# Kernel tuning notes

Measured on AMD Instinct MI355X. Metric: run time of the kernel, lower is better.

## Reference

```python
import jax, jax.numpy as jnp
import numpy as np

B, D, DM, K, KA = 4096, 64, 256, 32, 16


def setup_inputs() -> dict:
    key = jax.random.key(0)
    ks = jax.random.split(key, 20)
    rn = lambda i, shape, s=1.0: jax.random.normal(ks[i], shape, dtype=jnp.float32) * s
    return dict(
        z=rn(0, (B, D)),
        rw=jax.random.uniform(ks[1], (B, K), dtype=jnp.float32),
        action_z=rn(2, (B, D)),
        action_rw=jax.random.uniform(ks[3], (B, KA), dtype=jnp.float32),
        action_code_z=rn(4, (B, D)),
        control=rn(5, (B, D)),
        exact_covector=rn(6, (B, D)),
        chart_emb=rn(7, (K, DM), 0.05),
        chart_anchor=rn(8, (K, D)),
        action_chart_emb=rn(9, (KA, DM), 0.05),
        action_chart_anchor=rn(10, (KA, D)),
        z_embed_W=rn(11, (D, DM), 0.05), z_embed_b=jnp.zeros((DM,), jnp.float32),
        lat_W=rn(12, (D, DM), 0.05), lat_b=jnp.zeros((DM,), jnp.float32),
        code_W=rn(13, (D, DM), 0.05), code_b=jnp.zeros((DM,), jnp.float32),
        Wq=rn(14, (DM, DM), 0.05), Wk=rn(15, (DM, DM), 0.05),
        Wv=rn(16, (DM, DM), 0.05), Wo=rn(17, (DM, DM), 0.05),
        form_W=rn(18, (DM, D), 0.05), form_b=jnp.zeros((D,), jnp.float32),
    )


def _spectral_linear(x, W, b):
    # SpectralLinear: weight normalized by its largest singular value.
    sigma = jnp.linalg.svd(W, compute_uv=False)[0]
    return x @ (W / jnp.maximum(sigma, jnp.float32(1e-8))) + b


def _forward(z, rw, action_z, action_rw, action_code_z, control, exact_covector,
             chart_emb, chart_anchor, action_chart_emb, action_chart_anchor,
             z_embed_W, z_embed_b, lat_W, lat_b, code_W, code_b,
             Wq, Wk, Wv, Wo, form_W, form_b):
    b = z.shape[0]
    # ChartTokenizer: routing-weighted chart embeddings + anchor latents.
    chart_x = rw[:, :, None] * chart_emb[None]                      # [B,K,DM]
    chart_z = jnp.broadcast_to(chart_anchor[None], (b, K, D))       # [B,K,D]
    a_chart_x = action_rw[:, :, None] * action_chart_emb[None]      # [B,KA,DM]
    a_chart_z = jnp.broadcast_to(action_chart_anchor[None], (b, KA, D))
    # LatentTokenizers: single token per latent.
    lat_x = (action_z @ lat_W + lat_b)[:, None, :]                  # [B,1,DM]
    code_x = (action_code_z @ code_W + code_b)[:, None, :]          # [B,1,DM]
    ctx_x = jnp.concatenate([lat_x, code_x, a_chart_x, chart_x], axis=1)   # [B,S,DM]
    ctx_z = jnp.concatenate([action_z[:, None], action_code_z[:, None], a_chart_z, chart_z], axis=1)  # [B,S,D]
    # CovariantAttention (1 head): feature scores biased by latent-space distance.
    x_q = z @ z_embed_W + z_embed_b                                 # [B,DM]
    q = x_q @ Wq                                                    # [B,DM]
    k = jnp.einsum('bsd,de->bse', ctx_x, Wk)                        # [B,S,DM]
    v = jnp.einsum('bsd,de->bse', ctx_x, Wv)
    dist2 = jnp.sum((z[:, None, :] - ctx_z) ** 2, axis=-1)          # [B,S]
    scores = jnp.einsum('bd,bsd->bs', q, k) / jnp.sqrt(jnp.float32(DM)) - dist2
    attn = jax.nn.softmax(scores, axis=-1)
    feat = jnp.einsum('bs,bsd->bd', attn, v) @ Wo                   # [B,DM]
    # Residual reward one-form, projected off the (detached) exact direction.
    form_raw = _spectral_linear(feat, form_W, form_b)               # [B,D]
    e = jax.lax.stop_gradient(exact_covector)
    e_norm2 = jnp.sum(e * e, axis=-1, keepdims=True)
    coeff = jnp.where(e_norm2 > 1e-8,
                      jnp.sum(form_raw * e, axis=-1, keepdims=True) / jnp.maximum(e_norm2, 1e-8),
                      jnp.zeros_like(e_norm2))
    form_cov = form_raw - coeff * e
    # Non-conservative scalar reward contribution.
    return jnp.sum(form_cov * control, axis=-1, keepdims=True)      # [B,1]


def reference(z, rw, action_z, action_rw, action_code_z, control, exact_covector,
              chart_emb, chart_anchor, action_chart_emb, action_chart_anchor,
              z_embed_W, z_embed_b, lat_W, lat_b, code_W, code_b,
              Wq, Wk, Wv, Wo, form_W, form_b):
    return _forward(z, rw, action_z, action_rw, action_code_z, control, exact_covector,
                    chart_emb, chart_anchor, action_chart_emb, action_chart_anchor,
                    z_embed_W, z_embed_b, lat_W, lat_b, code_W, code_b,
                    Wq, Wk, Wv, Wo, form_W, form_b)
```

## Files before the change

### kernel.cpp

```cpp
#include <hip/hip_runtime.h>

#define PITERS 96

#define OFF_XQ   0
#define OFF_KL   16640
#define OFF_KC   33280
#define OFF_VL   49920
#define OFF_VC   66560
#define OFF_KE   83200
#define OFF_VE   95488
#define OFF_M    107776
#define OFF_G    124160
#define OFF_PLm  128256
#define OFF_PLc  132416
#define OFF_PCm  132488
#define OFF_PCc  136648
#define OFF_CK2  136720
#define OFF_ANCT 139840
#define OFF_ANCN 142912
#define OFF_VM   142976
#define OFF_LM   146048
#define OFF_CM   150208
#define OFF_RS   154368

__device__ __forceinline__ float wred(float v) {
  #pragma unroll
  for (int m = 32; m >= 1; m >>= 1) v += __shfl_xor(v, m, 64);
  return v;
}

__global__ __launch_bounds__(256)
void k1a(const float* __restrict__ chemb, const float* __restrict__ aemb,
         const float* __restrict__ zW, const float* __restrict__ zb,
         const float* __restrict__ latW, const float* __restrict__ latb,
         const float* __restrict__ codeW, const float* __restrict__ codeb,
         const float* __restrict__ Wq, const float* __restrict__ Wk,
         const float* __restrict__ Wv, const float* __restrict__ Wo,
         const float* __restrict__ fW, float* __restrict__ ws) {
  __shared__ __align__(16) float red[1024];
  const int t = threadIdx.x, b = blockIdx.x;
  const int j = t & 63, ks = t >> 6;

  const float *a0p, *a1p, *a2p, *a3p;
  const float* Bm;
  int bstride = 256, jbase = 0;
  int d0, d1, d2, d3;
  bool gpath = false;

  if (b < 340) {
    int u = b / 68, r2 = b - u * 68;
    int rg = r2 >> 2, jc = r2 & 3; jbase = jc * 64;
    const float *Wmat, *bias;
    if (u == 0)      { Wmat = zW;    bias = zb;    Bm = Wq; }
    else if (u == 1) { Wmat = latW;  bias = latb;  Bm = Wk; }
    else if (u == 2) { Wmat = codeW; bias = codeb; Bm = Wk; }
    else if (u == 3) { Wmat = latW;  bias = latb;  Bm = Wv; }
    else             { Wmat = codeW; bias = codeb; Bm = Wv; }
    int r0 = rg * 4;
    int rr0 = r0 + 0, rr1 = r0 + 1, rr2 = r0 + 2, rr3 = r0 + 3;
    a0p = (rr0 < 64) ? (Wmat + rr0 * 256) : bias;
    a1p = (rr1 <= 64) ? ((rr1 < 64) ? (Wmat + rr1 * 256) : bias) : bias;
    a2p = (rr2 <= 64) ? ((rr2 < 64) ? (Wmat + rr2 * 256) : bias) : bias;
    a3p = (rr3 <= 64) ? ((rr3 < 64) ? (Wmat + rr3 * 256) : bias) : bias;
    d0 = u * 16640 + rr0 * 256 + jbase;
    d1 = (rr1 <= 64) ? (u * 16640 + rr1 * 256 + jbase) : -1;
    d2 = (rr2 <= 64) ? (u * 16640 + rr2 * 256 + jbase) : -1;
    d3 = (rr3 <= 64) ? (u * 16640 + rr3 * 256 + jbase) : -1;
  } else if (b < 436) {
    int b2 = b - 340; int isV = (b2 >= 48); int rr = b2 - (isV ? 48 : 0);
    int rg = rr >> 2, jc = rr & 3; jbase = jc * 64;
    Bm = isV ? Wv : Wk;
    int base = isV ? OFF_VE : OFF_KE;
    int s0 = rg * 4;
    const float* e0 = (s0 + 0 < 16) ? (aemb + (s0 + 0) * 256) : (chemb + (s0 + 0 - 16) * 256);
    const float* e1 = (s0 + 1 < 16) ? (aemb + (s0 + 1) * 256) : (chemb + (s0 + 1 - 16) * 256);
    const float* e2 = (s0 + 2 < 16) ? (aemb + (s0 + 2) * 256) : (chemb + (s0 + 2 - 16) * 256);
    const float* e3 = (s0 + 3 < 16) ? (aemb + (s0 + 3) * 256) : (chemb + (s0 + 3 - 16) * 256);
    a0p = e0; a1p = e1; a2p = e2; a3p = e3;
    d0 = base + (s0 + 0) * 256 + jbase;
    d1 = base + (s0 + 1) * 256 + jbase;
    d2 = base + (s0 + 2) * 256 + jbase;
    d3 = base + (s0 + 3) * 256 + jbase;
  } else if (b < 500) {
    int i0 = (b - 436) * 4;
    Bm = fW; bstride = 64;
    a0p = Wo + (i0 + 0) * 256; a1p = Wo + (i0 + 1) * 256;
    a2p = Wo + (i0 + 2) * 256; a3p = Wo + (i0 + 3) * 256;
    d0 = OFF_M + (i0 + 0) * 64; d1 = OFF_M + (i0 + 1) * 64;
    d2 = OFF_M + (i0 + 2) * 64; d3 = OFF_M + (i0 + 3) * 64;
  } else {
    gpath = true;
    int i0 = (b - 500) * 4;
    Bm = fW; bstride = 64;
    a0p = fW + i0 + 0; a1p = fW + i0 + 1; a2p = fW + i0 + 2; a3p = fW + i0 + 3;
    d0 = OFF_G + (i0 + 0) * 64; d1 = OFF_G + (i0 + 1) * 64;
    d2 = OFF_G + (i0 + 2) * 64; d3 = OFF_G + (i0 + 3) * 64;
  }

  float acc0 = 0.f, acc1 = 0.f, acc2 = 0.f, acc3 = 0.f;
  const float* bp = Bm + (ks * 64) * bstride + jbase + j;
  if (!gpath) {
    const float* a0 = a0p + ks * 64;
    const float* a1 = a1p + ks * 64;
    const float* a2 = a2p + ks * 64;
    const float* a3 = a3p + ks * 64;
    #pragma unroll 4
    for (int k4 = 0; k4 < 16; ++k4) {
      float b0 = bp[(k4 * 4 + 0) * bstride];
      float b1 = bp[(k4 * 4 + 1) * bstride];
      float b2 = bp[(k4 * 4 + 2) * bstride];
      float b3 = bp[(k4 * 4 + 3) * bstride];
      float4 x0 = *(const float4*)(a0 + k4 * 4);
      float4 x1 = *(const float4*)(a1 + k4 * 4);
      float4 x2 = *(const float4*)(a2 + k4 * 4);
      float4 x3 = *(const float4*)(a3 + k4 * 4);
      acc0 += x0.x * b0 + x0.y * b1 + x0.z * b2 + x0.w * b3;
      acc1 += x1.x * b0 + x1.y * b1 + x1.z * b2 + x1.w * b3;
      acc2 += x2.x * b0 + x2.y * b1 + x2.z * b2 + x2.w * b3;
      acc3 += x3.x * b0 + x3.y * b1 + x3.z * b2 + x3.w * b3;
    }
  } else {
    const float* a0 = a0p + (ks * 64) * 64;
    const float* a1 = a1p + (ks * 64) * 64;
    const float* a2 = a2p + (ks * 64) * 64;
    const float* a3 = a3p + (ks * 64) * 64;
    #pragma unroll 4
    for (int k = 0; k < 64; ++k) {
      float bv = bp[k * bstride];
      acc0 += a0[k * 64] * bv;
      acc1 += a1[k * 64] * bv;
      acc2 += a2[k * 64] * bv;
      acc3 += a3[k * 64] * bv;
    }
  }
  red[0 * 256 + t] = acc0;
  red[1 * 256 + t] = acc1;
  red[2 * 256 + t] = acc2;
  red[3 * 256 + t] = acc3;
  __syncthreads();
  if (t < 64) {
    if (d0 >= 0) ws[d0 + t] = (red[t] + red[64 + t]) + (red[128 + t] + red[192 + t]);
    if (d1 >= 0) ws[d1 + t] = (red[256 + t] + red[320 + t]) + (red[384 + t] + red[448 + t]);
    if (d2 >= 0) ws[d2 + t] = (red[512 + t] + red[576 + t]) + (red[640 + t] + red[704 + t]);
    if (d3 >= 0) ws[d3 + t] = (red[768 + t] + red[832 + t]) + (red[896 + t] + red[960 + t]);
  }
}

__global__ __launch_bounds__(256)
void k1b(const float* __restrict__ latb, const float* __restrict__ codeb,
         const float* __restrict__ aanc, const float* __restrict__ chanc,
         float* __restrict__ ws) {
  __shared__ __align__(16) float red[256];
  const int t = threadIdx.x, b = blockIdx.x;

  if (b == 0) {
    if (t >= 64) return;
    const int ln = t;
    float4 h[16];
    #pragma unroll
    for (int k4 = 0; k4 < 16; ++k4)
      h[k4] = *(const float4*)(ws + OFF_G + ln * 64 + k4 * 4);
    float rn = 0.f;
    #pragma unroll
    for (int k4 = 0; k4 < 16; ++k4)
      rn += h[k4].x * h[k4].x + h[k4].y * h[k4].y + h[k4].z * h[k4].z + h[k4].w * h[k4].w;
    float bv = rn; int bj = ln;
    #pragma unroll
    for (int m = 32; m >= 1; m >>= 1) {
      float ov = __shfl_xor(bv, m, 64);
      int   oj = __shfl_xor(bj, m, 64);
      if (ov > bv || (ov == bv && oj < bj)) { bv = ov; bj = oj; }
    }
    float v = ws[OFF_G + bj * 64 + ln];
    for (int it = 0; it < PITERS; ++it) {
      red[ln] = v;
      float y0 = 0.f, y1 = 0.f, y2 = 0.f, y3 = 0.f;
      #pragma unroll
      for (int k4 = 0; k4 < 16; ++k4) {
        float4 vv = *(const float4*)&red[k4 * 4];
        y0 = fmaf(h[k4].x, vv.x, y0);
        y1 = fmaf(h[k4].y, vv.y, y1);
        y2 = fmaf(h[k4].z, vv.z, y2);
        y3 = fmaf(h[k4].w, vv.w, y3);
      }
      float y = (y0 + y1) + (y2 + y3);
      if ((it & 7) == 7) {
        float n2 = wred(y * y);
        y = (n2 > 0.f) ? y * rsqrtf(n2) : 0.f;
      }
      v = y;
    }
    red[ln] = v;
    float y0 = 0.f, y1 = 0.f, y2 = 0.f, y3 = 0.f;
    #pragma unroll
    for (int k4 = 0; k4 < 16; ++k4) {
      float4 vv = *(const float4*)&red[k4 * 4];
      y0 = fmaf(h[k4].x, vv.x, y0);
      y1 = fmaf(h[k4].y, vv.y, y1);
      y2 = fmaf(h[k4].z, vv.z, y2);
      y3 = fmaf(h[k4].w, vv.w, y3);
    }
    float y = (y0 + y1) + (y2 + y3);
    float num = wred(v * y), den = wred(v * v);
    if (ln == 0) {
      float lam = (den > 1e-37f) ? num / den : 0.f;
      lam = fmaxf(lam, 0.f);
      ws[OFF_RS] = 1.f / fmaxf(sqrtf(lam), 1e-8f);
    }
    return;
  }

  const int q = b - 1;

  if (q == 374) {
    for (int e = t; e < 3072; e += 256) {
      int d = e / 48, s = e - d * 48;
      const float* a = (s < 16) ? (aanc + s * 64) : (chanc + (s - 16) * 64);
      ws[OFF_ANCT + e] = a[d];
    }
    if (t < 64) {
      float n = 0.f;
      if (t < 48) {
        const float* a = (t < 16) ? (aanc + t * 64) : (chanc + (t - 16) * 64);
        #pragma unroll 4
        for (int d = 0; d < 64; ++d) n += a[d] * a[d];
      }
      ws[OFF_ANCN + t] = n;
    }
    return;
  }
  if (q == 373) {
    if (t < 65) {
      const float* ap = ws + OFF_XQ + t * 256;
      const float* bp = ws + OFF_KL + 64 * 256;
      float acc = 0.f;
      #pragma unroll 4
      for (int e = 0; e < 256; ++e) acc += ap[e] * bp[e];
      ws[OFF_PLc + t] = acc;
    } else if (t >= 128 && t < 193) {
      int r = t - 128;
      const float* ap = ws + OFF_XQ + r * 256;
      const float* bp = ws + OFF_KC + 64 * 256;
      float acc = 0.f;
      #pragma unroll 4
      for (int e = 0; e < 256; ++e) acc += ap[e] * bp[e];
      ws[OFF_PCc + r] = acc;
    }
    return;
  }

  const int j = t & 63, ks = t >> 6;
  const float* ap; const float* bp;
  int bstride, dstBase, nout = 64;
  if (q < 325) {
    int g = q / 65, r = q - g * 65;
    const float* A = ws + ((g < 3) ? OFF_XQ : (g == 3 ? OFF_VL : OFF_VC)) + r * 256;
    if (g == 0)      { bp = ws + OFF_KL + j * 256 + ks * 64; bstride = 1; dstBase = OFF_PLm + r * 64; }
    else if (g == 1) { bp = ws + OFF_KC + j * 256 + ks * 64; bstride = 1; dstBase = OFF_PCm + r * 64; }
    else if (g == 2) { int jj = (j < 48) ? j : 47;
                       bp = ws + OFF_KE + jj * 256 + ks * 64; bstride = 1; dstBase = OFF_CK2 + r * 48; nout = 48; }
    else if (g == 3) { bp = ws + OFF_M + (ks * 64) * 64 + j; bstride = 64; dstBase = OFF_LM + r * 64; }
    else             { bp = ws + OFF_M + (ks * 64) * 64 + j; bstride = 64; dstBase = OFF_CM + r * 64; }
    ap = A + ks * 64;
  } else {
    int s = q - 325;
    ap = ws + OFF_VE + s * 256 + ks * 64;
    bp = ws + OFF_M + (ks * 64) * 64 + j; bstride = 64;
    dstBase = OFF_VM + s * 64;
  }
  float a0 = 0.f, a1 = 0.f, a2 = 0.f, a3 = 0.f;
  #pragma unroll 4
  for (int k = 0; k < 64; k += 4) {
    a0 += ap[k + 0] * bp[(k + 0) * bstride];
    a1 += ap[k + 1] * bp[(k + 1) * bstride];
    a2 += ap[k + 2] * bp[(k + 2) * bstride];
    a3 += ap[k + 3] * bp[(k + 3) * bstride];
  }
  red[t] = (a0 + a1) + (a2 + a3);
  __syncthreads();
  if (t < nout) ws[dstBase + t] = red[t] + red[64 + t] + red[128 + t] + red[192 + t];
}

__global__ __launch_bounds__(256)
void k2_main(const float* __restrict__ z, const float* __restrict__ rw,
             const float* __restrict__ az, const float* __restrict__ arw,
             const float* __restrict__ acz, const float* __restrict__ ctrl,
             const float* __restrict__ ecov, const float* __restrict__ fb,
             const float* __restrict__ ws, float* __restrict__ out) {
  const int t = threadIdx.x;
  const int wv = t >> 6, ln = t & 63;

  const int bb = blockIdx.x * 8 + wv * 2;
  float z0 = z[bb * 64 + ln],        z1 = z[(bb + 1) * 64 + ln];
  float a0 = az[bb * 64 + ln],       a1 = az[(bb + 1) * 64 + ln];
  float c0 = acz[bb * 64 + ln],      c1 = acz[(bb + 1) * 64 + ln];
  float cc0 = ctrl[bb * 64 + ln],    cc1 = ctrl[(bb + 1) * 64 + ln];
  float ee0 = ecov[bb * 64 + ln],    ee1 = ecov[(bb + 1) * 64 + ln];
  float fbv = fb[ln];
  const float rs = ws[OFF_RS];
  float fold0 = 1.f, fold1 = 1.f;
  if (ln < 16)      { fold0 = arw[bb * 16 + ln];        fold1 = arw[(bb + 1) * 16 + ln]; }
  else if (ln < 48) { fold0 = rw[bb * 32 + (ln - 16)];  fold1 = rw[(bb + 1) * 32 + (ln - 16)]; }

  float dL0 = wred((z0 - a0) * (z0 - a0));
  float dL1 = wred((z1 - a1) * (z1 - a1));
  float dC0 = wred((z0 - c0) * (z0 - c0));
  float dC1 = wred((z1 - c1) * (z1 - c1));
  float zn0 = wred(z0 * z0);
  float zn1 = wred(z1 * z1);

  const float* plm = ws + OFF_PLm + ln;
  const float* pcm = ws + OFF_PCm + ln;
  float uL0 = plm[64 * 64], uL1 = uL0;
  float uC0 = pcm[64 * 64], uC1 = uC0;
  #pragma unroll 8
  for (int k = 0; k < 64; ++k) {
    float pm = plm[k * 64], pc = pcm[k * 64];
    float zk0 = __shfl(z0, k, 64), zk1 = __shfl(z1, k, 64);
    uL0 = fmaf(zk0, pm, uL0); uL1 = fmaf(zk1, pm, uL1);
    uC0 = fmaf(zk0, pc, uC0); uC1 = fmaf(zk1, pc, uC1);
  }
  float plc = ws[OFF_PLc + ln], pcc = ws[OFF_PCc + ln];
  float plcc = ws[OFF_PLc + 64], pccc = ws[OFF_PCc + 64];
  float sL0 = wred(uL0 * a0 + z0 * plc) + plcc;
  float sL1 = wred(uL1 * a1 + z1 * plc) + plcc;
  float sC0 = wred(uC0 * c0 + z0 * pcc) + pccc;
  float sC1 = wred(uC1 * c1 + z1 * pcc) + pccc;
  float scl0 = sL0 * 0.0625f - dL0, scl1 = sL1 * 0.0625f - dL1;
  float scc0 = sC0 * 0.0625f - dC0, scc1 = sC1 * 0.0625f - dC1;

  const float* ck = ws + OFF_CK2 + ln;
  const float* an = ws + OFF_ANCT + ln;
  float ca0 = ck[64 * 48], ca1 = ca0;
  float za0 = 0.f, za1 = 0.f;
  #pragma unroll 8
  for (int k = 0; k < 64; ++k) {
    float cv = ck[k * 48], av = an[k * 48];
    float zk0 = __shfl(z0, k, 64), zk1 = __shfl(z1, k, 64);
    ca0 = fmaf(zk0, cv, ca0); ca1 = fmaf(zk1, cv, ca1);
    za0 = fmaf(zk0, av, za0); za1 = fmaf(zk1, av, za1);
  }
  float ancn = ws[OFF_ANCN + ln];
  float sc0 = fold0 * ca0 * 0.0625f - (zn0 - 2.f * za0 + ancn);
  float sc1 = fold1 * ca1 * 0.0625f - (zn1 - 2.f * za1 + ancn);
  if (ln == 48) { sc0 = scl0; sc1 = scl1; }
  if (ln == 49) { sc0 = scc0; sc1 = scc1; }
  if (ln > 49)  { sc0 = -1e30f; sc1 = -1e30f; }

  float mx0 = sc0, mx1 = sc1;
  #pragma unroll
  for (int m = 32; m >= 1; m >>= 1) {
    mx0 = fmaxf(mx0, __shfl_xor(mx0, m, 64));
    mx1 = fmaxf(mx1, __shfl_xor(mx1, m, 64));
  }
  float ev0 = (ln < 50) ? __expf(sc0 - mx0) : 0.f;
  float ev1 = (ln < 50) ? __expf(sc1 - mx1) : 0.f;
  float sum0 = wred(ev0), sum1 = wred(ev1);
  float w0 = ev0 * (1.f / sum0) * fold0;
  float w1 = ev1 * (1.f / sum1) * fold1;

  float g0 = 0.f, g1 = 0.f;
  const float* vm = ws + OFF_VM + ln;
  #pragma unroll 8
  for (int s = 0; s < 48; ++s) {
    float vvv = vm[s * 64];
    float s0 = __shfl(w0, s, 64), s1 = __shfl(w1, s, 64);
    g0 = fmaf(s0, vvv, g0); g1 = fmaf(s1, vvv, g1);
  }
  const float* lm = ws + OFF_LM + ln;
  const float* cm = ws + OFF_CM + ln;
  float l0 = lm[64 * 64], l1 = l0;
  float m0 = cm[64 * 64], m1 = m0;
  #pragma unroll 8
  for (int k = 0; k < 64; ++k) {
    float lv = lm[k * 64], cv = cm[k * 64];
    float ak0 = __shfl(a0, k, 64), ak1 = __shfl(a1, k, 64);
    float qk0 = __shfl(c0, k, 64), qk1 = __shfl(c1, k, 64);
    l0 = fmaf(ak0, lv, l0); l1 = fmaf(ak1, lv, l1);
    m0 = fmaf(qk0, cv, m0); m1 = fmaf(qk1, cv, m1);
  }
  float w48_0 = __shfl(w0, 48, 64), w49_0 = __shfl(w0, 49, 64);
  float w48_1 = __shfl(w1, 48, 64), w49_1 = __shfl(w1, 49, 64);
  g0 += w48_0 * l0 + w49_0 * m0;
  g1 += w48_1 * l1 + w49_1 * m1;

  #pragma unroll
  for (int s = 0; s < 2; ++s) {
    float g  = (s == 0) ? g0 : g1;
    float cc = (s == 0) ? cc0 : cc1;
    float ee = (s == 0) ? ee0 : ee1;
    int bbs  = bb + s;
    float gc = wred(g * cc);
    float ge = wred(g * ee);
    float ec = wred(ee * cc);
    float en = wred(ee * ee);
    float fc = wred(fbv * cc);
    float fe = wred(fbv * ee);
    if (ln == 0) {
      float A, Bv;
      if (en > 1e-8f) { float r = ec / en; A = gc - ge * r; Bv = fc - fe * r; }
      else { A = gc; Bv = fc; }
      out[bbs] = A * rs + Bv;
    }
  }
}

extern "C" void kernel_launch(void* const* d_in, const int* in_sizes, int n_in,
                              void* d_out, int out_size, void* d_ws, size_t ws_size,
                              hipStream_t stream) {
  const float* z     = (const float*)d_in[0];
  const float* rw    = (const float*)d_in[1];
  const float* az    = (const float*)d_in[2];
  const float* arw   = (const float*)d_in[3];
  const float* acz   = (const float*)d_in[4];
  const float* ctrl  = (const float*)d_in[5];
  const float* ecov  = (const float*)d_in[6];
  const float* chemb = (const float*)d_in[7];
  const float* chanc = (const float*)d_in[8];
  const float* aemb  = (const float*)d_in[9];
  const float* aanc  = (const float*)d_in[10];
  const float* zW    = (const float*)d_in[11];
  const float* zb    = (const float*)d_in[12];
  const float* latW  = (const float*)d_in[13];
  const float* latb  = (const float*)d_in[14];
  const float* codeW = (const float*)d_in[15];
  const float* codeb = (const float*)d_in[16];
  const float* Wq    = (const float*)d_in[17];
  const float* Wk    = (const float*)d_in[18];
  const float* Wv    = (const float*)d_in[19];
  const float* Wo    = (const float*)d_in[20];
  const float* fW    = (const float*)d_in[21];
  const float* fb    = (const float*)d_in[22];
  float* ws  = (float*)d_ws;
  float* out = (float*)d_out;

  k1a<<<516, 256, 0, stream>>>(chemb, aemb, zW, zb, latW, latb, codeW, codeb,
                               Wq, Wk, Wv, Wo, fW, ws);
  k1b<<<376, 256, 0, stream>>>(latb, codeb, aanc, chanc, ws);
  k2_main<<<512, 256, 0, stream>>>(z, rw, az, arw, acz, ctrl, ecov, fb, ws, out);
}
```

Measured before the change: 172.8 us.

## Compute spectral norm via repeated Gram squaring in one block, fewer power iterations

The Gram matrix fW^T fW is now computed inside a single k1a block in shared memory and then squared five times with trace normalisation, so the power method runs on G^32. That lets the power iteration drop from 96 steps to 6. The serial power-iteration block moves out of k1b into k1a, and the OFF_G workspace round trip disappears. The cost is that one k1a block now does several 64x64 matmuls serially and uses about 52KB of shared memory, which may lower occupancy for every k1a block. Accuracy now depends on the repeated squaring converging well.

```diff
diff --git a/kernel.cpp b/kernel.cpp
--- a/kernel.cpp
+++ b/kernel.cpp
@@ -1,6 +1,6 @@
 #include <hip/hip_runtime.h>
 
-#define PITERS 96
+#define PITERS 6
 
 #define OFF_XQ   0
 #define OFF_KL   16640
@@ -10,7 +10,6 @@
 #define OFF_KE   83200
 #define OFF_VE   95488
 #define OFF_M    107776
-#define OFF_G    124160
 #define OFF_PLm  128256
 #define OFF_PLc  132416
 #define OFF_PCm  132488
@@ -37,16 +36,152 @@
          const float* __restrict__ Wq, const float* __restrict__ Wk,
          const float* __restrict__ Wv, const float* __restrict__ Wo,
          const float* __restrict__ fW, float* __restrict__ ws) {
-  __shared__ __align__(16) float red[1024];
+  __shared__ __align__(16) float sm[13120];
   const int t = threadIdx.x, b = blockIdx.x;
+
+  if (b == 500) {
+    const int ln = t & 63;
+    float* bufA = sm;
+    float* G0   = sm + 4352;
+    float* bufB = sm + 8704;
+    float* red  = sm + 13056;
+    const int ty = t >> 4, tx = t & 15;
+    const int i0 = ty * 4, j0 = tx * 4;
+    float acc[4][4];
+    #pragma unroll
+    for (int i = 0; i < 4; ++i)
+      #pragma unroll
+      for (int j = 0; j < 4; ++j) acc[i][j] = 0.f;
+    for (int c = 0; c < 4; ++c) {
+      if (c) __syncthreads();
+      for (int e = t; e < 4096; e += 256) {
+        int k = e >> 6, i = e & 63;
+        bufA[i * 68 + k] = fW[(c * 64 + k) * 64 + i];
+      }
+      __syncthreads();
+      #pragma unroll 4
+      for (int k4 = 0; k4 < 16; ++k4) {
+        float4 av[4], bv[4];
+        #pragma unroll
+        for (int i = 0; i < 4; ++i) av[i] = *(const float4*)&bufA[(i0 + i) * 68 + k4 * 4];
+        #pragma unroll
+        for (int j = 0; j < 4; ++j) bv[j] = *(const float4*)&bufA[(j0 + j) * 68 + k4 * 4];
+        #pragma unroll
+        for (int i = 0; i < 4; ++i)
+          #pragma unroll
+          for (int j = 0; j < 4; ++j)
+            acc[i][j] += av[i].x * bv[j].x + av[i].y * bv[j].y + av[i].z * bv[j].z + av[i].w * bv[j].w;
+      }
+    }
+    if (ty == tx) red[ty] = acc[0][0] + acc[1][1] + acc[2][2] + acc[3][3];
+    __syncthreads();
+    {
+      float tr = 0.f;
+      #pragma unroll
+      for (int x = 0; x < 16; ++x) tr += red[x];
+      float inv = (tr > 0.f) ? 1.f / tr : 0.f;
+      #pragma unroll
+      for (int i = 0; i < 4; ++i) {
+        *(float4*)&G0[(i0 + i) * 68 + j0]   = make_float4(acc[i][0], acc[i][1], acc[i][2], acc[i][3]);
+        *(float4*)&bufB[(i0 + i) * 68 + j0] = make_float4(acc[i][0] * inv, acc[i][1] * inv,
+                                                          acc[i][2] * inv, acc[i][3] * inv);
+      }
+    }
+    __syncthreads();
+    float* src = bufB;
+    float* dst = bufA;
+    for (int sq = 0; sq < 5; ++sq) {
+      #pragma unroll
+      for (int i = 0; i < 4; ++i)
+        #pragma unroll
+        for (int j = 0; j < 4; ++j) acc[i][j] = 0.f;
+      #pragma unroll 4
+      for (int k4 = 0; k4 < 16; ++k4) {
+        float4 av[4], bv[4];
+        #pragma unroll
+        for (int i = 0; i < 4; ++i) av[i] = *(const float4*)&src[(i0 + i) * 68 + k4 * 4];
+        #pragma unroll
+        for (int j = 0; j < 4; ++j) bv[j] = *(const float4*)&src[(j0 + j) * 68 + k4 * 4];
+        #pragma unroll
+        for (int i = 0; i < 4; ++i)
+          #pragma unroll
+          for (int j = 0; j < 4; ++j)
+            acc[i][j] += av[i].x * bv[j].x + av[i].y * bv[j].y + av[i].z * bv[j].z + av[i].w * bv[j].w;
+      }
+      if (ty == tx) red[ty] = acc[0][0] + acc[1][1] + acc[2][2] + acc[3][3];
+      __syncthreads();
+      {
+        float tr = 0.f;
+        #pragma unroll
+        for (int x = 0; x < 16; ++x) tr += red[x];
+        float inv = (tr > 0.f) ? 1.f / tr : 0.f;
+        #pragma unroll
+        for (int i = 0; i < 4; ++i)
+          *(float4*)&dst[(i0 + i) * 68 + j0] = make_float4(acc[i][0] * inv, acc[i][1] * inv,
+                                                           acc[i][2] * inv, acc[i][3] * inv);
+      }
+      __syncthreads();
+      float* tmp = src; src = dst; dst = tmp;
+    }
+    if (t < 64) {
+      float4 h[16];
+      #pragma unroll
+      for (int k4 = 0; k4 < 16; ++k4) h[k4] = *(const float4*)&src[ln * 68 + k4 * 4];
+      float rn = 0.f;
+      #pragma unroll
+      for (int k4 = 0; k4 < 16; ++k4)
+        rn += h[k4].x * h[k4].x + h[k4].y * h[k4].y + h[k4].z * h[k4].z + h[k4].w * h[k4].w;
+      float bnv = rn; int bj = ln;
+      #pragma unroll
+      for (int m = 32; m >= 1; m >>= 1) {
+        float ov = __shfl_xor(bnv, m, 64);
+        int   oj = __shfl_xor(bj, m, 64);
+        if (ov > bnv || (ov == bnv && oj < bj)) { bnv = ov; bj = oj; }
+      }
+      float v = src[bj * 68 + ln];
+      for (int pi = 0; pi < PITERS; ++pi) {
+        red[ln] = v;
+        float y0 = 0.f, y1 = 0.f, y2 = 0.f, y3 = 0.f;
+        #pragma unroll
+        for (int k4 = 0; k4 < 16; ++k4) {
+          float4 vvv = *(const float4*)&red[k4 * 4];
+          y0 = fmaf(h[k4].x, vvv.x, y0);
+          y1 = fmaf(h[k4].y, vvv.y, y1);
+          y2 = fmaf(h[k4].z, vvv.z, y2);
+          y3 = fmaf(h[k4].w, vvv.w, y3);
+        }
+        float y = (y0 + y1) + (y2 + y3);
+        float n2 = wred(y * y);
+        v = (n2 > 0.f) ? y * rsqrtf(n2) : 0.f;
+      }
+      red[ln] = v;
+      float y0 = 0.f, y1 = 0.f, y2 = 0.f, y3 = 0.f;
+      #pragma unroll
+      for (int k4 = 0; k4 < 16; ++k4) {
+        float4 gg = *(const float4*)&G0[ln * 68 + k4 * 4];
+        float4 vvv = *(const float4*)&red[k4 * 4];
+        y0 = fmaf(gg.x, vvv.x, y0);
+        y1 = fmaf(gg.y, vvv.y, y1);
+        y2 = fmaf(gg.z, vvv.z, y2);
+        y3 = fmaf(gg.w, vvv.w, y3);
+      }
+      float y = (y0 + y1) + (y2 + y3);
+      float num = wred(v * y), den = wred(v * v);
+      if (ln == 0) {
+        float lam = (den > 1e-37f) ? num / den : 0.f;
+        lam = fmaxf(lam, 0.f);
+        ws[OFF_RS] = 1.f / fmaxf(sqrtf(lam), 1e-8f);
+      }
+    }
+    return;
+  }
+
+  float* red = sm;
   const int j = t & 63, ks = t >> 6;
-
   const float *a0p, *a1p, *a2p, *a3p;
   const float* Bm;
   int bstride = 256, jbase = 0;
   int d0, d1, d2, d3;
-  bool gpath = false;
-
   if (b < 340) {
     int u = b / 68, r2 = b - u * 68;
     int rg = r2 >> 2, jc = r2 & 3; jbase = jc * 64;
@@ -57,12 +192,12 @@
     else if (u == 3) { Wmat = latW;  bias = latb;  Bm = Wv; }
     else             { Wmat = codeW; bias = codeb; Bm = Wv; }
     int r0 = rg * 4;
-    int rr0 = r0 + 0, rr1 = r0 + 1, rr2 = r0 + 2, rr3 = r0 + 3;
-    a0p = (rr0 < 64) ? (Wmat + rr0 * 256) : bias;
-    a1p = (rr1 <= 64) ? ((rr1 < 64) ? (Wmat + rr1 * 256) : bias) : bias;
-    a2p = (rr2 <= 64) ? ((rr2 < 64) ? (Wmat + rr2 * 256) : bias) : bias;
-    a3p = (rr3 <= 64) ? ((rr3 < 64) ? (Wmat + rr3 * 256) : bias) : bias;
-    d0 = u * 16640 + rr0 * 256 + jbase;
+    int rr1 = r0 + 1, rr2 = r0 + 2, rr3 = r0 + 3;
+    a0p = (r0 < 64) ? (Wmat + r0 * 256) : bias;
+    a1p = (rr1 < 64) ? (Wmat + rr1 * 256) : bias;
+    a2p = (rr2 < 64) ? (Wmat + rr2 * 256) : bias;
+    a3p = (rr3 < 64) ? (Wmat + rr3 * 256) : bias;
+    d0 = u * 16640 + r0 * 256 + jbase;
     d1 = (rr1 <= 64) ? (u * 16640 + rr1 * 256 + jbase) : -1;
     d2 = (rr2 <= 64) ? (u * 16640 + rr2 * 256 + jbase) : -1;
     d3 = (rr3 <= 64) ? (u * 16640 + rr3 * 256 + jbase) : -1;
@@ -72,66 +207,42 @@
     Bm = isV ? Wv : Wk;
     int base = isV ? OFF_VE : OFF_KE;
     int s0 = rg * 4;
-    const float* e0 = (s0 + 0 < 16) ? (aemb + (s0 + 0) * 256) : (chemb + (s0 + 0 - 16) * 256);
-    const float* e1 = (s0 + 1 < 16) ? (aemb + (s0 + 1) * 256) : (chemb + (s0 + 1 - 16) * 256);
-    const float* e2 = (s0 + 2 < 16) ? (aemb + (s0 + 2) * 256) : (chemb + (s0 + 2 - 16) * 256);
-    const float* e3 = (s0 + 3 < 16) ? (aemb + (s0 + 3) * 256) : (chemb + (s0 + 3 - 16) * 256);
-    a0p = e0; a1p = e1; a2p = e2; a3p = e3;
+    a0p = (s0 + 0 < 16) ? (aemb + (s0 + 0) * 256) : (chemb + (s0 + 0 - 16) * 256);
+    a1p = (s0 + 1 < 16) ? (aemb + (s0 + 1) * 256) : (chemb + (s0 + 1 - 16) * 256);
+    a2p = (s0 + 2 < 16) ? (aemb + (s0 + 2) * 256) : (chemb + (s0 + 2 - 16) * 256);
+    a3p = (s0 + 3 < 16) ? (aemb + (s0 + 3) * 256) : (chemb + (s0 + 3 - 16) * 256);
     d0 = base + (s0 + 0) * 256 + jbase;
     d1 = base + (s0 + 1) * 256 + jbase;
     d2 = base + (s0 + 2) * 256 + jbase;
     d3 = base + (s0 + 3) * 256 + jbase;
-  } else if (b < 500) {
+  } else {
     int i0 = (b - 436) * 4;
     Bm = fW; bstride = 64;
     a0p = Wo + (i0 + 0) * 256; a1p = Wo + (i0 + 1) * 256;
     a2p = Wo + (i0 + 2) * 256; a3p = Wo + (i0 + 3) * 256;
     d0 = OFF_M + (i0 + 0) * 64; d1 = OFF_M + (i0 + 1) * 64;
     d2 = OFF_M + (i0 + 2) * 64; d3 = OFF_M + (i0 + 3) * 64;
-  } else {
-    gpath = true;
-    int i0 = (b - 500) * 4;
-    Bm = fW; bstride = 64;
-    a0p = fW + i0 + 0; a1p = fW + i0 + 1; a2p = fW + i0 + 2; a3p = fW + i0 + 3;
-    d0 = OFF_G + (i0 + 0) * 64; d1 = OFF_G + (i0 + 1) * 64;
-    d2 = OFF_G + (i0 + 2) * 64; d3 = OFF_G + (i0 + 3) * 64;
-  }
-
+  }
   float acc0 = 0.f, acc1 = 0.f, acc2 = 0.f, acc3 = 0.f;
   const float* bp = Bm + (ks * 64) * bstride + jbase + j;
-  if (!gpath) {
-    const float* a0 = a0p + ks * 64;
-    const float* a1 = a1p + ks * 64;
-    const float* a2 = a2p + ks * 64;
-    const float* a3 = a3p + ks * 64;
-    #pragma unroll 4
-    for (int k4 = 0; k4 < 16; ++k4) {
-      float b0 = bp[(k4 * 4 + 0) * bstride];
-      float b1 = bp[(k4 * 4 + 1) * bstride];
-      float b2 = bp[(k4 * 4 + 2) * bstride];
-      float b3 = bp[(k4 * 4 + 3) * bstride];
-      float4 x0 = *(const float4*)(a0 + k4 * 4);
-      float4 x1 = *(const float4*)(a1 + k4 * 4);
-      float4 x2 = *(const float4*)(a2 + k4 * 4);
-      float4 x3 = *(const float4*)(a3 + k4 * 4);
-      acc0 += x0.x * b0 + x0.y * b1 + x0.z * b2 + x0.w * b3;
-      acc1 += x1.x * b0 + x1.y * b1 + x1.z * b2 + x1.w * b3;
-      acc2 += x2.x * b0 + x2.y * b1 + x2.z * b2 + x2.w * b3;
-      acc3 += x3.x * b0 + x3.y * b1 + x3.z * b2 + x3.w * b3;
-    }
-  } else {
-    const float* a0 = a0p + (ks * 64) * 64;
-    const float* a1 = a1p + (ks * 64) * 64;
-    const float* a2 = a2p + (ks * 64) * 64;
-    const float* a3 = a3p + (ks * 64) * 64;
-    #pragma unroll 4
-    for (int k = 0; k < 64; ++k) {
-      float bv = bp[k * bstride];
-      acc0 += a0[k * 64] * bv;
-      acc1 += a1[k * 64] * bv;
-      acc2 += a2[k * 64] * bv;
-      acc3 += a3[k * 64] * bv;
-    }
+  const float* a0 = a0p + ks * 64;
+  const float* a1 = a1p + ks * 64;
+  const float* a2 = a2p + ks * 64;
+  const float* a3 = a3p + ks * 64;
+  #pragma unroll 4
+  for (int k4 = 0; k4 < 16; ++k4) {
+    float b0 = bp[(k4 * 4 + 0) * bstride];
+    float b1 = bp[(k4 * 4 + 1) * bstride];
+    float b2 = bp[(k4 * 4 + 2) * bstride];
+    float b3 = bp[(k4 * 4 + 3) * bstride];
+    float4 x0 = *(const float4*)(a0 + k4 * 4);
+    float4 x1 = *(const float4*)(a1 + k4 * 4);
+    float4 x2 = *(const float4*)(a2 + k4 * 4);
+    float4 x3 = *(const float4*)(a3 + k4 * 4);
+    acc0 += x0.x * b0 + x0.y * b1 + x0.z * b2 + x0.w * b3;
+    acc1 += x1.x * b0 + x1.y * b1 + x1.z * b2 + x1.w * b3;
+    acc2 += x2.x * b0 + x2.y * b1 + x2.z * b2 + x2.w * b3;
+    acc3 += x3.x * b0 + x3.y * b1 + x3.z * b2 + x3.w * b3;
   }
   red[0 * 256 + t] = acc0;
   red[1 * 256 + t] = acc1;
@@ -150,67 +261,8 @@
 void k1b(const float* __restrict__ latb, const float* __restrict__ codeb,
          const float* __restrict__ aanc, const float* __restrict__ chanc,
          float* __restrict__ ws) {
-  __shared__ __align__(16) float red[256];
-  const int t = threadIdx.x, b = blockIdx.x;
-
-  if (b == 0) {
-    if (t >= 64) return;
-    const int ln = t;
-    float4 h[16];
-    #pragma unroll
-    for (int k4 = 0; k4 < 16; ++k4)
-      h[k4] = *(const float4*)(ws + OFF_G + ln * 64 + k4 * 4);
-    float rn = 0.f;
-    #pragma unroll
-    for (int k4 = 0; k4 < 16; ++k4)
-      rn += h[k4].x * h[k4].x + h[k4].y * h[k4].y + h[k4].z * h[k4].z + h[k4].w * h[k4].w;
-    float bv = rn; int bj = ln;
-    #pragma unroll
-    for (int m = 32; m >= 1; m >>= 1) {
-      float ov = __shfl_xor(bv, m, 64);
-      int   oj = __shfl_xor(bj, m, 64);
-      if (ov > bv || (ov == bv && oj < bj)) { bv = ov; bj = oj; }
-    }
-    float v = ws[OFF_G + bj * 64 + ln];
-    for (int it = 0; it < PITERS; ++it) {
-      red[ln] = v;
-      float y0 = 0.f, y1 = 0.f, y2 = 0.f, y3 = 0.f;
-      #pragma unroll
-      for (int k4 = 0; k4 < 16; ++k4) {
-        float4 vv = *(const float4*)&red[k4 * 4];
-        y0 = fmaf(h[k4].x, vv.x, y0);
-        y1 = fmaf(h[k4].y, vv.y, y1);
-        y2 = fmaf(h[k4].z, vv.z, y2);
-        y3 = fmaf(h[k4].w, vv.w, y3);
-      }
-      float y = (y0 + y1) + (y2 + y3);
-      if ((it & 7) == 7) {
-        float n2 = wred(y * y);
-        y = (n2 > 0.f) ? y * rsqrtf(n2) : 0.f;
-      }
-      v = y;
-    }
-    red[ln] = v;
-    float y0 = 0.f, y1 = 0.f, y2 = 0.f, y3 = 0.f;
-    #pragma unroll
-    for (int k4 = 0; k4 < 16; ++k4) {
-      float4 vv = *(const float4*)&red[k4 * 4];
-      y0 = fmaf(h[k4].x, vv.x, y0);
-      y1 = fmaf(h[k4].y, vv.y, y1);
-      y2 = fmaf(h[k4].z, vv.z, y2);
-      y3 = fmaf(h[k4].w, vv.w, y3);
-    }
-    float y = (y0 + y1) + (y2 + y3);
-    float num = wred(v * y), den = wred(v * v);
-    if (ln == 0) {
-      float lam = (den > 1e-37f) ? num / den : 0.f;
-      lam = fmaxf(lam, 0.f);
-      ws[OFF_RS] = 1.f / fmaxf(sqrtf(lam), 1e-8f);
-    }
-    return;
-  }
-
-  const int q = b - 1;
+  __shared__ float red[256];
+  const int t = threadIdx.x, q = blockIdx.x;
 
   if (q == 374) {
     for (int e = t; e < 3072; e += 256) {
@@ -434,8 +486,8 @@
   float* ws  = (float*)d_ws;
   float* out = (float*)d_out;
 
-  k1a<<<516, 256, 0, stream>>>(chemb, aemb, zW, zb, latW, latb, codeW, codeb,
+  k1a<<<501, 256, 0, stream>>>(chemb, aemb, zW, zb, latW, latb, codeW, codeb,
                                Wq, Wk, Wv, Wo, fW, ws);
-  k1b<<<376, 256, 0, stream>>>(latb, codeb, aanc, chanc, ws);
+  k1b<<<375, 256, 0, stream>>>(latb, codeb, aanc, chanc, ws);
   k2_main<<<512, 256, 0, stream>>>(z, rw, az, arw, acz, ctrl, ecov, fb, ws, out);
 }
```

Result: slower. 185.3 us (+7.2%).
